# Performance work log

Measured on AMD Instinct MI355X. Metric: run time of the kernel, lower is better.

The kernel has to match this reference:

```python
import jax, jax.numpy as jnp
import numpy as np

N_NODES = 100000
N_GRAPHS = 512
HID = 128
IN_DIM = 128
OUT_DIM = 10
N_EDGES = 1600000


def gcn_conv(x, src, dst, W, b, n):
    # PyG GCNConv: add self-loops, symmetric normalization D^-1/2 (A+I) D^-1/2, then linear.
    h = x @ W  # [N, H]
    deg = jnp.zeros((n,), h.dtype).at[dst].add(1.0) + 1.0  # +1 self-loop
    dinv = jax.lax.rsqrt(deg)
    norm = dinv[src] * dinv[dst]  # [E]
    agg = jnp.zeros_like(h).at[dst].add(h[src] * norm[:, None])
    agg = agg + h * (dinv * dinv)[:, None]  # self-loop messages
    return agg + b


def setup_inputs() -> dict:
    key = jax.random.key(0)
    ks = jax.random.split(key, 12)
    x = jax.random.normal(ks[0], (N_NODES, IN_DIM), jnp.float32)
    edge_index = jax.random.randint(ks[1], (2, N_EDGES), 0, N_NODES)
    batch = jnp.sort(jax.random.randint(ks[2], (N_NODES,), 0, N_GRAPHS))
    def lin(k, fan_in, shape):
        bound = 1.0 / np.sqrt(fan_in)
        return jax.random.uniform(k, shape, jnp.float32, -bound, bound)
    W1 = lin(ks[3], IN_DIM, (IN_DIM, HID)); b1 = lin(ks[4], IN_DIM, (HID,))
    W2 = lin(ks[5], HID, (HID, HID)); b2 = lin(ks[6], HID, (HID,))
    W3 = lin(ks[7], HID, (HID, HID)); b3 = lin(ks[8], HID, (HID,))
    Wc1 = lin(ks[9], 2 * HID, (2 * HID, HID)); bc1 = lin(ks[9], 2 * HID, (HID,))
    Wc2 = lin(ks[10], HID, (HID, OUT_DIM)); bc2 = lin(ks[11], HID, (OUT_DIM,))
    return {"x": x, "edge_index": edge_index, "batch": batch,
            "W1": W1, "b1": b1, "W2": W2, "b2": b2, "W3": W3, "b3": b3,
            "Wc1": Wc1, "bc1": bc1, "Wc2": Wc2, "bc2": bc2}


def reference(x, edge_index, batch, W1, b1, W2, b2, W3, b3, Wc1, bc1, Wc2, bc2):
    src, dst = edge_index[0], edge_index[1]
    n = x.shape[0]
    h = jax.nn.relu(gcn_conv(x, src, dst, W1, b1, n))
    h = jax.nn.relu(gcn_conv(h, src, dst, W2, b2, n))
    h = gcn_conv(h, src, dst, W3, b3, n)  # no relu after last conv
    # global mean pool
    sums = jax.ops.segment_sum(h, batch, num_segments=N_GRAPHS)
    cnt = jax.ops.segment_sum(jnp.ones((n,), h.dtype), batch, num_segments=N_GRAPHS)
    mean = sums / jnp.maximum(cnt, 1.0)[:, None]
    # global max pool
    mx = jax.ops.segment_max(h, batch, num_segments=N_GRAPHS)
    mx = jnp.where(jnp.isfinite(mx), mx, 0.0)
    g = jnp.concatenate([mean, mx], axis=1)  # [G, 2H]
    g = jax.nn.relu(g @ Wc1 + bc1)
    return g @ Wc2 + bc2
```

## Files before the change

### kernel.cpp

```cpp
#include <hip/hip_runtime.h>

#define H 128
#define CAP 64
#define NB 256
#define BPCAP 6144
#define EPB 8192

typedef __attribute__((ext_vector_type(8))) short bf16x8;
typedef __attribute__((ext_vector_type(4))) float f32x4;

__device__ __forceinline__ unsigned short f2bf(float f) {
  unsigned u = __float_as_uint(f);
  unsigned r = u + 0x7FFFu + ((u >> 16) & 1u);
  return (unsigned short)(r >> 16);
}
__device__ __forceinline__ float bf2f(unsigned short s) {
  return __uint_as_float(((unsigned)s) << 16);
}

__global__ __launch_bounds__(256) void setup_all(
    const float* __restrict__ x,
    const float* __restrict__ W1, const float* __restrict__ W2, const float* __restrict__ W3,
    unsigned short* __restrict__ Xb, unsigned short* __restrict__ Wt,
    const int* __restrict__ batch, int* __restrict__ g_start, int G,
    unsigned short* __restrict__ P, unsigned short* __restrict__ Q,
    int* __restrict__ bcount,
    int n, int totalX4) {
  long long i = (long long)blockIdx.x * 256 + threadIdx.x;
  if (i < totalX4) {
    float4 v = *(const float4*)(x + i * 4);
    ushort4 o;
    o.x = f2bf(v.x); o.y = f2bf(v.y); o.z = f2bf(v.z); o.w = f2bf(v.w);
    *(ushort4*)(Xb + i * 4) = o;
    return;
  }
  i -= totalX4;
  if (i < 3 * H * H) {
    int w = (int)(i >> 14);
    int rem = (int)i & (H * H - 1);
    int c = rem >> 7;
    int k = rem & 127;
    const float* W = (w == 0) ? W1 : (w == 1) ? W2 : W3;
    Wt[i] = f2bf(W[(size_t)k * H + c]);
    return;
  }
  i -= 3 * H * H;
  if (i < n) {
    int ii = (int)i;
    int b = batch[ii];
    int prev = (ii == 0) ? -1 : batch[ii - 1];
    for (int g = prev + 1; g <= b; ++g) g_start[g] = ii;
    if (ii == n - 1) {
      for (int g = b + 1; g <= G; ++g) g_start[g] = n;
    }
    return;
  }
  i -= n;
  if (i < H) {
    P[(size_t)n * H + i] = 0;
    Q[(size_t)n * H + i] = 0;
    return;
  }
  i -= H;
  if (i < 512) bcount[i] = 0;
}

__global__ __launch_bounds__(256) void split1(
    const int* __restrict__ src, const int* __restrict__ dst,
    int2* __restrict__ buckets, int* __restrict__ bcount,
    int ne, int nbuck) {
  __shared__ int cnt[512];
  __shared__ int gbase[512];
  int tid = threadIdx.x;
  for (int i = tid; i < 512; i += 256) cnt[i] = 0;
  __syncthreads();

  int beg = blockIdx.x * EPB;
  int end = beg + EPB; if (end > ne) end = ne;

  for (int e = beg + tid; e < end; e += 256) {
    int d = dst[e];
    atomicAdd(&cnt[d >> 8], 1);
  }
  __syncthreads();
  for (int i = tid; i < nbuck; i += 256) {
    int c = cnt[i];
    gbase[i] = (c > 0) ? atomicAdd(&bcount[i], c) : 0;
    cnt[i] = 0;
  }
  __syncthreads();
  for (int e = beg + tid; e < end; e += 256) {
    int s = src[e];
    int d = dst[e];
    int b = d >> 8;
    int l = atomicAdd(&cnt[b], 1);
    int pos = gbase[b] + l;
    if (pos < BPCAP) buckets[(size_t)b * BPCAP + pos] = make_int2(s, d);
  }
}

__global__ __launch_bounds__(256) void build_csr(
    const int2* __restrict__ buckets, const int* __restrict__ bcount,
    int* __restrict__ csr_src, int* __restrict__ deg, float* __restrict__ dinv,
    int n) {
  __shared__ int cur[NB];
  int b = blockIdx.x;
  int tid = threadIdx.x;
  cur[tid] = 0;
  __syncthreads();
  int cntb = bcount[b]; if (cntb > BPCAP) cntb = BPCAP;
  const int2* bp = buckets + (size_t)b * BPCAP;
  for (int i = tid; i < cntb; i += 256) {
    int2 e = bp[i];
    int slot = atomicAdd(&cur[e.y & (NB - 1)], 1);
    if (slot < CAP) csr_src[(size_t)e.y * CAP + slot] = e.x;
  }
  __syncthreads();
  int node = b * NB + tid;
  if (node < n) {
    int d = cur[tid];
    deg[node] = d;
    dinv[node] = rsqrtf((float)(d + 1));
  }
}

#define SWLD 136
__global__ __launch_bounds__(256) void gemm_mfma(
    const unsigned short* __restrict__ Ab, const unsigned short* __restrict__ Wt,
    const float* __restrict__ dinv, unsigned short* __restrict__ outb, int n) {
  __shared__ unsigned short sW[H * SWLD];
  int tid = threadIdx.x;
  {
    int c = tid >> 1, hh = tid & 1;
    const int4* s = (const int4*)(Wt + (size_t)c * H + hh * 64);
    int4* d = (int4*)(sW + (size_t)c * SWLD + hh * 64);
#pragma unroll
    for (int i = 0; i < 8; ++i) d[i] = s[i];
  }
  __syncthreads();

  int wave = tid >> 6;
  int lane = tid & 63;
  int m = lane & 15;
  int quad = lane >> 4;
  int row = blockIdx.x * 64 + wave * 16 + m;
  bool rv = row < n;

  f32x4 acc[8];
#pragma unroll
  for (int t = 0; t < 8; ++t) acc[t] = (f32x4){0.f, 0.f, 0.f, 0.f};

  const unsigned short* arow = Ab + (size_t)(rv ? row : 0) * H;
#pragma unroll
  for (int k0 = 0; k0 < H; k0 += 32) {
    bf16x8 af;
    if (rv) af = *(const bf16x8*)(arow + k0 + quad * 8);
    else    af = (bf16x8){0, 0, 0, 0, 0, 0, 0, 0};
#pragma unroll
    for (int ct = 0; ct < 8; ++ct) {
      bf16x8 bfr = *(const bf16x8*)(sW + (size_t)(ct * 16 + m) * SWLD + k0 + quad * 8);
      acc[ct] = __builtin_amdgcn_mfma_f32_16x16x32_bf16(af, bfr, acc[ct], 0, 0, 0);
    }
  }

  int orow0 = blockIdx.x * 64 + wave * 16 + quad * 4;
#pragma unroll
  for (int r = 0; r < 4; ++r) {
    int orow = orow0 + r;
    if (orow < n) {
      float dv = dinv[orow];
      unsigned short* o = outb + (size_t)orow * H + m;
#pragma unroll
      for (int ct = 0; ct < 8; ++ct) o[ct * 16] = f2bf(acc[ct][r] * dv);
    }
  }
}

template <bool RELU, bool OUTF32>
__global__ __launch_bounds__(256) void aggregate_bf(
    const unsigned short* __restrict__ hs, const int* __restrict__ deg_,
    const int* __restrict__ csr_src, const float* __restrict__ dinv,
    const float* __restrict__ b, void* __restrict__ outv, int n) {
  int node = blockIdx.x * 8 + (threadIdx.x >> 5);
  if (node >= n) return;
  int c = (threadIdx.x & 31) << 2;
  int deg = deg_[node]; if (deg > CAP) deg = CAP;
  int beg = node * CAP;
  int end = beg + ((deg + 7) & ~7);

  ushort4 sv = *(const ushort4*)(hs + (size_t)node * H + c);
  float4 acc;
  acc.x = bf2f(sv.x); acc.y = bf2f(sv.y); acc.z = bf2f(sv.z); acc.w = bf2f(sv.w);

  int4 ia, ib;
  if (beg < end) {
    ia = *(const int4*)(csr_src + beg);
    ib = *(const int4*)(csr_src + beg + 4);
  }
  for (int k = beg; k < end; k += 8) {
    int4 ca = ia, cb = ib;
    int kn = k + 8;
    if (kn < end) {
      ia = *(const int4*)(csr_src + kn);
      ib = *(const int4*)(csr_src + kn + 4);
    }
    int rk = k - beg;
    if (rk + 8 > deg) {
      ca.x = (rk + 0 < deg) ? ca.x : n;
      ca.y = (rk + 1 < deg) ? ca.y : n;
      ca.z = (rk + 2 < deg) ? ca.z : n;
      ca.w = (rk + 3 < deg) ? ca.w : n;
      cb.x = (rk + 4 < deg) ? cb.x : n;
      cb.y = (rk + 5 < deg) ? cb.y : n;
      cb.z = (rk + 6 < deg) ? cb.z : n;
      cb.w = (rk + 7 < deg) ? cb.w : n;
    }
    ushort4 v0 = *(const ushort4*)(hs + (size_t)ca.x * H + c);
    ushort4 v1 = *(const ushort4*)(hs + (size_t)ca.y * H + c);
    ushort4 v2 = *(const ushort4*)(hs + (size_t)ca.z * H + c);
    ushort4 v3 = *(const ushort4*)(hs + (size_t)ca.w * H + c);
    ushort4 v4 = *(const ushort4*)(hs + (size_t)cb.x * H + c);
    ushort4 v5 = *(const ushort4*)(hs + (size_t)cb.y * H + c);
    ushort4 v6 = *(const ushort4*)(hs + (size_t)cb.z * H + c);
    ushort4 v7 = *(const ushort4*)(hs + (size_t)cb.w * H + c);
    acc.x += ((bf2f(v0.x) + bf2f(v1.x)) + (bf2f(v2.x) + bf2f(v3.x))) +
             ((bf2f(v4.x) + bf2f(v5.x)) + (bf2f(v6.x) + bf2f(v7.x)));
    acc.y += ((bf2f(v0.y) + bf2f(v1.y)) + (bf2f(v2.y) + bf2f(v3.y))) +
             ((bf2f(v4.y) + bf2f(v5.y)) + (bf2f(v6.y) + bf2f(v7.y)));
    acc.z += ((bf2f(v0.z) + bf2f(v1.z)) + (bf2f(v2.z) + bf2f(v3.z))) +
             ((bf2f(v4.z) + bf2f(v5.z)) + (bf2f(v6.z) + bf2f(v7.z)));
    acc.w += ((bf2f(v0.w) + bf2f(v1.w)) + (bf2f(v2.w) + bf2f(v3.w))) +
             ((bf2f(v4.w) + bf2f(v5.w)) + (bf2f(v6.w) + bf2f(v7.w)));
  }

  float dv = dinv[node];
  float4 bb = *(const float4*)(b + c);
  float4 o;
  o.x = fmaf(acc.x, dv, bb.x);
  o.y = fmaf(acc.y, dv, bb.y);
  o.z = fmaf(acc.z, dv, bb.z);
  o.w = fmaf(acc.w, dv, bb.w);
  if (RELU) {
    o.x = fmaxf(o.x, 0.f); o.y = fmaxf(o.y, 0.f);
    o.z = fmaxf(o.z, 0.f); o.w = fmaxf(o.w, 0.f);
  }
  if (OUTF32) {
    *(float4*)((float*)outv + (size_t)node * H + c) = o;
  } else {
    ushort4 ob;
    ob.x = f2bf(o.x); ob.y = f2bf(o.y); ob.z = f2bf(o.z); ob.w = f2bf(o.w);
    *(ushort4*)((unsigned short*)outv + (size_t)node * H + c) = ob;
  }
}

__global__ __launch_bounds__(256) void pool2(
    const float* __restrict__ h, const int* __restrict__ g_start,
    float* __restrict__ gmean, float* __restrict__ gmax, int n) {
  __shared__ float ssum[16][64];
  __shared__ float smax[16][64];
  int g = blockIdx.x >> 1;
  int half = blockIdx.x & 1;
  int beg = g_start[g];
  int end = g_start[g + 1];
  int q = threadIdx.x >> 4;
  int c = (threadIdx.x & 15) << 2;
  int cg = half * 64 + c;

  float4 s = make_float4(0.f, 0.f, 0.f, 0.f);
  float4 m = make_float4(-INFINITY, -INFINITY, -INFINITY, -INFINITY);
  for (int node = beg + q; node < end; node += 16) {
    float4 v = *(const float4*)(h + (size_t)node * H + cg);
    s.x += v.x; s.y += v.y; s.z += v.z; s.w += v.w;
    m.x = fmaxf(m.x, v.x); m.y = fmaxf(m.y, v.y);
    m.z = fmaxf(m.z, v.z); m.w = fmaxf(m.w, v.w);
  }
  *(float4*)&ssum[q][c] = s;
  *(float4*)&smax[q][c] = m;
  __syncthreads();

  int cnt = end - beg;
  int t = threadIdx.x;
  if (t < 64) {
    float tot = 0.f;
#pragma unroll
    for (int qq = 0; qq < 16; ++qq) tot += ssum[qq][t];
    gmean[(size_t)g * H + half * 64 + t] = tot / fmaxf((float)cnt, 1.0f);
  } else if (t < 128) {
    int cc = t - 64;
    float mx = -INFINITY;
#pragma unroll
    for (int qq = 0; qq < 16; ++qq) mx = fmaxf(mx, smax[qq][cc]);
    gmax[(size_t)g * H + half * 64 + cc] = (cnt == 0) ? 0.0f : mx;
  }
}

__global__ __launch_bounds__(128) void classify_kernel(
    const float* __restrict__ gmean, const float* __restrict__ gmax,
    const float* __restrict__ Wc1, const float* __restrict__ bc1,
    const float* __restrict__ Wc2, const float* __restrict__ bc2,
    float* __restrict__ out) {
  __shared__ float gv[2 * H];
  __shared__ float hid[H];
  int gid = blockIdx.x;
  int t = threadIdx.x;
  gv[t] = gmean[(size_t)gid * H + t];
  gv[H + t] = gmax[(size_t)gid * H + t];
  __syncthreads();
  float acc = 0.f;
#pragma unroll 8
  for (int k = 0; k < 2 * H; ++k) acc = fmaf(gv[k], Wc1[(size_t)k * H + t], acc);
  hid[t] = fmaxf(acc + bc1[t], 0.f);
  __syncthreads();
  if (t < 10) {
    float a2 = 0.f;
    for (int j = 0; j < H; ++j) a2 = fmaf(hid[j], Wc2[(size_t)j * 10 + t], a2);
    out[(size_t)gid * 10 + t] = a2 + bc2[t];
  }
}

extern "C" void kernel_launch(void* const* d_in, const int* in_sizes, int n_in,
                              void* d_out, int out_size, void* d_ws, size_t ws_size,
                              hipStream_t stream) {
  const float* x    = (const float*)d_in[0];
  const int* ei     = (const int*)d_in[1];
  const int* batch  = (const int*)d_in[2];
  const float* W1   = (const float*)d_in[3];
  const float* b1   = (const float*)d_in[4];
  const float* W2   = (const float*)d_in[5];
  const float* b2   = (const float*)d_in[6];
  const float* W3   = (const float*)d_in[7];
  const float* b3   = (const float*)d_in[8];
  const float* Wc1  = (const float*)d_in[9];
  const float* bc1  = (const float*)d_in[10];
  const float* Wc2  = (const float*)d_in[11];
  const float* bc2  = (const float*)d_in[12];
  float* out = (float*)d_out;

  const int n  = in_sizes[2];
  const int ne = in_sizes[1] / 2;
  const int G  = 512;
  const size_t NFb = (size_t)(n + 1) * H;

  const int* src = ei;
  const int* dst = ei + ne;

  unsigned short* P_bf = (unsigned short*)d_ws;
  unsigned short* Q_bf = P_bf + NFb;
  float*          F2f  = (float*)(Q_bf + NFb);
  unsigned short* Xb   = (unsigned short*)F2f;
  int* csr_src = (int*)(F2f + (size_t)n * H);
  const size_t csr_cap = (size_t)n * CAP;
  char* p = (char*)(csr_src + csr_cap);
  int*            deg      = (int*)p;            p += (size_t)n * 4;
  float*          dinv     = (float*)p;          p += (size_t)n * 4;
  int*            g_start  = (int*)p;            p += (size_t)(G + 1) * 4;
  float*          gmean    = (float*)p;          p += (size_t)G * H * 4;
  float*          gmax     = (float*)p;          p += (size_t)G * H * 4;
  p = (char*)(((uintptr_t)p + 255) & ~(uintptr_t)255);
  unsigned short* Wt       = (unsigned short*)p; p += (size_t)3 * H * H * 2;
  int*            bcount   = (int*)p;            p += 512 * 4;
  int2*           buckets  = (int2*)Q_bf;

  const int nbuck = (n + NB - 1) / NB;

  {
    int totalX4 = n * H / 4;
    long long tot = (long long)totalX4 + 3 * H * H + n + H + 512;
    int blocks = (int)((tot + 255) / 256);
    setup_all<<<blocks, 256, 0, stream>>>(x, W1, W2, W3, Xb, Wt,
                                          batch, g_start, G,
                                          P_bf, Q_bf, bcount, n, totalX4);
  }

  split1<<<(ne + EPB - 1) / EPB, 256, 0, stream>>>(src, dst, buckets, bcount, ne, nbuck);
  build_csr<<<nbuck, 256, 0, stream>>>(buckets, bcount, csr_src, deg, dinv, n);

  const int tile_grid = (n + 63) / 64;
  const int node_grid = (n + 7) / 8;

  gemm_mfma<<<tile_grid, 256, 0, stream>>>(Xb, Wt, dinv, Q_bf, n);
  aggregate_bf<true, false><<<node_grid, 256, 0, stream>>>(Q_bf, deg, csr_src, dinv, b1, P_bf, n);

  gemm_mfma<<<tile_grid, 256, 0, stream>>>(P_bf, Wt + H * H, dinv, Q_bf, n);
  aggregate_bf<true, false><<<node_grid, 256, 0, stream>>>(Q_bf, deg, csr_src, dinv, b2, P_bf, n);

  gemm_mfma<<<tile_grid, 256, 0, stream>>>(P_bf, Wt + 2 * H * H, dinv, Q_bf, n);
  aggregate_bf<false, true><<<node_grid, 256, 0, stream>>>(Q_bf, deg, csr_src, dinv, b3, F2f, n);

  pool2<<<2 * G, 256, 0, stream>>>(F2f, g_start, gmean, gmax, n);
  classify_kernel<<<G, 128, 0, stream>>>(gmean, gmax, Wc1, bc1, Wc2, bc2, out);
}
```

Baseline: 432.0 us.

## Widen aggregation gathers to 16B, stage GEMM output in LDS, fuse pool+classify

Aggregation now assigns 16 threads per node with 8 bf16 channels each, loading 16-byte vectors per neighbor and unpacking bf16 pairs. This is meant to cut memory instruction count and improve gather efficiency. The GEMM epilogue writes results into shared memory and then emits coalesced 16-byte row stores instead of scattered 2-byte stores. Pooling and the classifier are merged into one kernel per graph, removing the intermediate buffers and a launch at the cost of fewer blocks for pooling.

```diff
diff --git a/kernel.cpp b/kernel.cpp
--- a/kernel.cpp
+++ b/kernel.cpp
@@ -8,14 +8,15 @@
 
 typedef __attribute__((ext_vector_type(8))) short bf16x8;
 typedef __attribute__((ext_vector_type(4))) float f32x4;
+typedef __attribute__((ext_vector_type(2))) float f32x2;
 
 __device__ __forceinline__ unsigned short f2bf(float f) {
   unsigned u = __float_as_uint(f);
   unsigned r = u + 0x7FFFu + ((u >> 16) & 1u);
   return (unsigned short)(r >> 16);
 }
-__device__ __forceinline__ float bf2f(unsigned short s) {
-  return __uint_as_float(((unsigned)s) << 16);
+__device__ __forceinline__ f32x2 up2(unsigned u) {
+  return (f32x2){__uint_as_float(u << 16), __uint_as_float(u & 0xFFFF0000u)};
 }
 
 __global__ __launch_bounds__(256) void setup_all(
@@ -163,15 +164,31 @@
     }
   }
 
-  int orow0 = blockIdx.x * 64 + wave * 16 + quad * 4;
+  __syncthreads();
+  unsigned short (*sOut)[136] = (unsigned short (*)[136])sW;
+  int r0 = wave * 16 + quad * 4;
 #pragma unroll
   for (int r = 0; r < 4; ++r) {
-    int orow = orow0 + r;
+    int orow = blockIdx.x * 64 + r0 + r;
+    float dv = (orow < n) ? dinv[orow] : 0.f;
+#pragma unroll
+    for (int ct = 0; ct < 8; ++ct)
+      sOut[r0 + r][ct * 16 + m] = f2bf(acc[ct][r] * dv);
+  }
+  __syncthreads();
+  {
+    int orow = blockIdx.x * 64 + (tid >> 2);
     if (orow < n) {
-      float dv = dinv[orow];
-      unsigned short* o = outb + (size_t)orow * H + m;
-#pragma unroll
-      for (int ct = 0; ct < 8; ++ct) o[ct * 16] = f2bf(acc[ct][r] * dv);
+      const unsigned short* sp = &sOut[tid >> 2][(tid & 3) * 32];
+      int4 t0 = *(const int4*)(sp + 0);
+      int4 t1 = *(const int4*)(sp + 8);
+      int4 t2 = *(const int4*)(sp + 16);
+      int4 t3 = *(const int4*)(sp + 24);
+      unsigned short* op = outb + (size_t)orow * H + (tid & 3) * 32;
+      *(int4*)(op + 0)  = t0;
+      *(int4*)(op + 8)  = t1;
+      *(int4*)(op + 16) = t2;
+      *(int4*)(op + 24) = t3;
     }
   }
 }
@@ -181,16 +198,15 @@
     const unsigned short* __restrict__ hs, const int* __restrict__ deg_,
     const int* __restrict__ csr_src, const float* __restrict__ dinv,
     const float* __restrict__ b, void* __restrict__ outv, int n) {
-  int node = blockIdx.x * 8 + (threadIdx.x >> 5);
+  int node = blockIdx.x * 16 + (threadIdx.x >> 4);
   if (node >= n) return;
-  int c = (threadIdx.x & 31) << 2;
+  int c = (threadIdx.x & 15) << 3;
   int deg = deg_[node]; if (deg > CAP) deg = CAP;
   int beg = node * CAP;
   int end = beg + ((deg + 7) & ~7);
 
-  ushort4 sv = *(const ushort4*)(hs + (size_t)node * H + c);
-  float4 acc;
-  acc.x = bf2f(sv.x); acc.y = bf2f(sv.y); acc.z = bf2f(sv.z); acc.w = bf2f(sv.w);
+  int4 sv = *(const int4*)(hs + (size_t)node * H + c);
+  f32x2 a0 = up2(sv.x), a1 = up2(sv.y), a2 = up2(sv.z), a3 = up2(sv.w);
 
   int4 ia, ib;
   if (beg < end) {
@@ -215,61 +231,68 @@
       cb.z = (rk + 6 < deg) ? cb.z : n;
       cb.w = (rk + 7 < deg) ? cb.w : n;
     }
-    ushort4 v0 = *(const ushort4*)(hs + (size_t)ca.x * H + c);
-    ushort4 v1 = *(const ushort4*)(hs + (size_t)ca.y * H + c);
-    ushort4 v2 = *(const ushort4*)(hs + (size_t)ca.z * H + c);
-    ushort4 v3 = *(const ushort4*)(hs + (size_t)ca.w * H + c);
-    ushort4 v4 = *(const ushort4*)(hs + (size_t)cb.x * H + c);
-    ushort4 v5 = *(const ushort4*)(hs + (size_t)cb.y * H + c);
-    ushort4 v6 = *(const ushort4*)(hs + (size_t)cb.z * H + c);
-    ushort4 v7 = *(const ushort4*)(hs + (size_t)cb.w * H + c);
-    acc.x += ((bf2f(v0.x) + bf2f(v1.x)) + (bf2f(v2.x) + bf2f(v3.x))) +
-             ((bf2f(v4.x) + bf2f(v5.x)) + (bf2f(v6.x) + bf2f(v7.x)));
-    acc.y += ((bf2f(v0.y) + bf2f(v1.y)) + (bf2f(v2.y) + bf2f(v3.y))) +
-             ((bf2f(v4.y) + bf2f(v5.y)) + (bf2f(v6.y) + bf2f(v7.y)));
-    acc.z += ((bf2f(v0.z) + bf2f(v1.z)) + (bf2f(v2.z) + bf2f(v3.z))) +
-             ((bf2f(v4.z) + bf2f(v5.z)) + (bf2f(v6.z) + bf2f(v7.z)));
-    acc.w += ((bf2f(v0.w) + bf2f(v1.w)) + (bf2f(v2.w) + bf2f(v3.w))) +
-             ((bf2f(v4.w) + bf2f(v5.w)) + (bf2f(v6.w) + bf2f(v7.w)));
+    int4 v0 = *(const int4*)(hs + (size_t)ca.x * H + c);
+    int4 v1 = *(const int4*)(hs + (size_t)ca.y * H + c);
+    int4 v2 = *(const int4*)(hs + (size_t)ca.z * H + c);
+    int4 v3 = *(const int4*)(hs + (size_t)ca.w * H + c);
+    int4 v4 = *(const int4*)(hs + (size_t)cb.x * H + c);
+    int4 v5 = *(const int4*)(hs + (size_t)cb.y * H + c);
+    int4 v6 = *(const int4*)(hs + (size_t)cb.z * H + c);
+    int4 v7 = *(const int4*)(hs + (size_t)cb.w * H + c);
+    a0 += ((up2(v0.x) + up2(v1.x)) + (up2(v2.x) + up2(v3.x))) +
+          ((up2(v4.x) + up2(v5.x)) + (up2(v6.x) + up2(v7.x)));
+    a1 += ((up2(v0.y) + up2(v1.y)) + (up2(v2.y) + up2(v3.y))) +
+          ((up2(v4.y) + up2(v5.y)) + (up2(v6.y) + up2(v7.y)));
+    a2 += ((up2(v0.z) + up2(v1.z)) + (up2(v2.z) + up2(v3.z))) +
+          ((up2(v4.z) + up2(v5.z)) + (up2(v6.z) + up2(v7.z)));
+    a3 += ((up2(v0.w) + up2(v1.w)) + (up2(v2.w) + up2(v3.w))) +
+          ((up2(v4.w) + up2(v5.w)) + (up2(v6.w) + up2(v7.w)));
   }
 
   float dv = dinv[node];
-  float4 bb = *(const float4*)(b + c);
-  float4 o;
-  o.x = fmaf(acc.x, dv, bb.x);
-  o.y = fmaf(acc.y, dv, bb.y);
-  o.z = fmaf(acc.z, dv, bb.z);
-  o.w = fmaf(acc.w, dv, bb.w);
+  float4 b0 = *(const float4*)(b + c);
+  float4 b1 = *(const float4*)(b + c + 4);
+  float o0 = fmaf(a0.x, dv, b0.x), o1 = fmaf(a0.y, dv, b0.y);
+  float o2 = fmaf(a1.x, dv, b0.z), o3 = fmaf(a1.y, dv, b0.w);
+  float o4 = fmaf(a2.x, dv, b1.x), o5 = fmaf(a2.y, dv, b1.y);
+  float o6 = fmaf(a3.x, dv, b1.z), o7 = fmaf(a3.y, dv, b1.w);
   if (RELU) {
-    o.x = fmaxf(o.x, 0.f); o.y = fmaxf(o.y, 0.f);
-    o.z = fmaxf(o.z, 0.f); o.w = fmaxf(o.w, 0.f);
+    o0 = fmaxf(o0, 0.f); o1 = fmaxf(o1, 0.f); o2 = fmaxf(o2, 0.f); o3 = fmaxf(o3, 0.f);
+    o4 = fmaxf(o4, 0.f); o5 = fmaxf(o5, 0.f); o6 = fmaxf(o6, 0.f); o7 = fmaxf(o7, 0.f);
   }
   if (OUTF32) {
-    *(float4*)((float*)outv + (size_t)node * H + c) = o;
+    float* fo = (float*)outv + (size_t)node * H + c;
+    *(float4*)(fo + 0) = make_float4(o0, o1, o2, o3);
+    *(float4*)(fo + 4) = make_float4(o4, o5, o6, o7);
   } else {
-    ushort4 ob;
-    ob.x = f2bf(o.x); ob.y = f2bf(o.y); ob.z = f2bf(o.z); ob.w = f2bf(o.w);
-    *(ushort4*)((unsigned short*)outv + (size_t)node * H + c) = ob;
-  }
-}
-
-__global__ __launch_bounds__(256) void pool2(
+    int4 ob;
+    ob.x = ((unsigned)f2bf(o1) << 16) | f2bf(o0);
+    ob.y = ((unsigned)f2bf(o3) << 16) | f2bf(o2);
+    ob.z = ((unsigned)f2bf(o5) << 16) | f2bf(o4);
+    ob.w = ((unsigned)f2bf(o7) << 16) | f2bf(o6);
+    *(int4*)((unsigned short*)outv + (size_t)node * H + c) = ob;
+  }
+}
+
+__global__ __launch_bounds__(256) void pool_classify(
     const float* __restrict__ h, const int* __restrict__ g_start,
-    float* __restrict__ gmean, float* __restrict__ gmax, int n) {
-  __shared__ float ssum[16][64];
-  __shared__ float smax[16][64];
-  int g = blockIdx.x >> 1;
-  int half = blockIdx.x & 1;
+    const float* __restrict__ Wc1, const float* __restrict__ bc1,
+    const float* __restrict__ Wc2, const float* __restrict__ bc2,
+    float* __restrict__ out) {
+  __shared__ float ssum[8][128];
+  __shared__ float smax[8][128];
+  __shared__ float gv[2 * H];
+  __shared__ float hid[H];
+  int g = blockIdx.x;
   int beg = g_start[g];
   int end = g_start[g + 1];
-  int q = threadIdx.x >> 4;
-  int c = (threadIdx.x & 15) << 2;
-  int cg = half * 64 + c;
+  int q = threadIdx.x >> 5;
+  int c = (threadIdx.x & 31) << 2;
 
   float4 s = make_float4(0.f, 0.f, 0.f, 0.f);
   float4 m = make_float4(-INFINITY, -INFINITY, -INFINITY, -INFINITY);
-  for (int node = beg + q; node < end; node += 16) {
-    float4 v = *(const float4*)(h + (size_t)node * H + cg);
+  for (int node = beg + q; node < end; node += 8) {
+    float4 v = *(const float4*)(h + (size_t)node * H + c);
     s.x += v.x; s.y += v.y; s.z += v.z; s.w += v.w;
     m.x = fmaxf(m.x, v.x); m.y = fmaxf(m.y, v.y);
     m.z = fmaxf(m.z, v.z); m.w = fmaxf(m.w, v.w);
@@ -280,41 +303,30 @@
 
   int cnt = end - beg;
   int t = threadIdx.x;
-  if (t < 64) {
+  if (t < 128) {
     float tot = 0.f;
 #pragma unroll
-    for (int qq = 0; qq < 16; ++qq) tot += ssum[qq][t];
-    gmean[(size_t)g * H + half * 64 + t] = tot / fmaxf((float)cnt, 1.0f);
-  } else if (t < 128) {
-    int cc = t - 64;
+    for (int qq = 0; qq < 8; ++qq) tot += ssum[qq][t];
+    gv[t] = tot / fmaxf((float)cnt, 1.0f);
+  } else {
+    int cc = t - 128;
     float mx = -INFINITY;
 #pragma unroll
-    for (int qq = 0; qq < 16; ++qq) mx = fmaxf(mx, smax[qq][cc]);
-    gmax[(size_t)g * H + half * 64 + cc] = (cnt == 0) ? 0.0f : mx;
-  }
-}
-
-__global__ __launch_bounds__(128) void classify_kernel(
-    const float* __restrict__ gmean, const float* __restrict__ gmax,
-    const float* __restrict__ Wc1, const float* __restrict__ bc1,
-    const float* __restrict__ Wc2, const float* __restrict__ bc2,
-    float* __restrict__ out) {
-  __shared__ float gv[2 * H];
-  __shared__ float hid[H];
-  int gid = blockIdx.x;
-  int t = threadIdx.x;
-  gv[t] = gmean[(size_t)gid * H + t];
-  gv[H + t] = gmax[(size_t)gid * H + t];
-  __syncthreads();
-  float acc = 0.f;
+    for (int qq = 0; qq < 8; ++qq) mx = fmaxf(mx, smax[qq][cc]);
+    gv[H + cc] = (cnt == 0) ? 0.0f : mx;
+  }
+  __syncthreads();
+  if (t < H) {
+    float acc = 0.f;
 #pragma unroll 8
-  for (int k = 0; k < 2 * H; ++k) acc = fmaf(gv[k], Wc1[(size_t)k * H + t], acc);
-  hid[t] = fmaxf(acc + bc1[t], 0.f);
+    for (int k = 0; k < 2 * H; ++k) acc = fmaf(gv[k], Wc1[(size_t)k * H + t], acc);
+    hid[t] = fmaxf(acc + bc1[t], 0.f);
+  }
   __syncthreads();
   if (t < 10) {
     float a2 = 0.f;
     for (int j = 0; j < H; ++j) a2 = fmaf(hid[j], Wc2[(size_t)j * 10 + t], a2);
-    out[(size_t)gid * 10 + t] = a2 + bc2[t];
+    out[(size_t)g * 10 + t] = a2 + bc2[t];
   }
 }
 
@@ -354,8 +366,6 @@
   int*            deg      = (int*)p;            p += (size_t)n * 4;
   float*          dinv     = (float*)p;          p += (size_t)n * 4;
   int*            g_start  = (int*)p;            p += (size_t)(G + 1) * 4;
-  float*          gmean    = (float*)p;          p += (size_t)G * H * 4;
-  float*          gmax     = (float*)p;          p += (size_t)G * H * 4;
   p = (char*)(((uintptr_t)p + 255) & ~(uintptr_t)255);
   unsigned short* Wt       = (unsigned short*)p; p += (size_t)3 * H * H * 2;
   int*            bcount   = (int*)p;            p += 512 * 4;
@@ -376,7 +386,7 @@
   build_csr<<<nbuck, 256, 0, stream>>>(buckets, bcount, csr_src, deg, dinv, n);
 
   const int tile_grid = (n + 63) / 64;
-  const int node_grid = (n + 7) / 8;
+  const int node_grid = (n + 15) / 16;
 
   gemm_mfma<<<tile_grid, 256, 0, stream>>>(Xb, Wt, dinv, Q_bf, n);
   aggregate_bf<true, false><<<node_grid, 256, 0, stream>>>(Q_bf, deg, csr_src, dinv, b1, P_bf, n);
@@ -387,6 +397,5 @@
   gemm_mfma<<<tile_grid, 256, 0, stream>>>(P_bf, Wt + 2 * H * H, dinv, Q_bf, n);
   aggregate_bf<false, true><<<node_grid, 256, 0, stream>>>(Q_bf, deg, csr_src, dinv, b3, F2f, n);
 
-  pool2<<<2 * G, 256, 0, stream>>>(F2f, g_start, gmean, gmax, n);
-  classify_kernel<<<G, 128, 0, stream>>>(gmean, gmax, Wc1, bc1, Wc2, bc2, out);
-}
+  pool_classify<<<G, 256, 0, stream>>>(F2f, g_start, Wc1, bc1, Wc2, bc2, out);
+}
```

After: 439.3 us. About the same (+1.7%).
